# Kernel tuning notes

Hardware: AMD Instinct MI355X
Metric: run time of the kernel (lower is better)

## Reference

```python
import jax, jax.numpy as jnp
import numpy as np
from jax import lax

V, E, H, NL, K = 32000, 1024, 1024, 3, 3
B, T = 16, 1024


def setup_inputs() -> dict:
    key = jax.random.key(0)
    ks = jax.random.split(key, 8)
    return {
        "input_ids": jax.random.randint(ks[0], (B, T), 0, V),
        "attention_mask": jnp.ones((B, T), dtype=jnp.int32),
        "emb": jax.random.normal(ks[1], (V, E), dtype=jnp.float32) * 0.02,
        "convW": jax.random.normal(ks[2], (NL, K, H, 3 * H), dtype=jnp.float32) * 0.02,
        "convb": jnp.zeros((NL, 3 * H), dtype=jnp.float32),
        "gamma": jnp.ones((NL, H), dtype=jnp.float32),
        "beta": jnp.zeros((NL, H), dtype=jnp.float32),
        "W1": jax.random.normal(ks[3], (H, H), dtype=jnp.float32) * 0.02,
        "b1": jnp.zeros((H,), dtype=jnp.float32),
        "W2": jax.random.normal(ks[4], (H, 2), dtype=jnp.float32) * 0.02,
        "b2": jnp.zeros((2,), dtype=jnp.float32),
    }


def _layer_norm(x, g, b, eps=1e-5):
    mu = x.mean(-1, keepdims=True)
    var = ((x - mu) ** 2).mean(-1, keepdims=True)
    return (x - mu) / jnp.sqrt(var + eps) * g + b


def _fo_pool(z, f, o, h0):
    # h_t = o_t * (f_t * h_{t-1} + (1-f_t) * z_t)  ->  h_t = a_t h_{t-1} + b_t
    a = o * f                      # [B,T,H]
    b = o * (1.0 - f) * z          # [B,T,H]
    b = b.at[:, 0].add(a[:, 0] * h0)  # fold initial hidden into first step
    def comb(x, y):
        a1, b1 = x
        a2, b2 = y
        return (a1 * a2, a2 * b1 + b2)
    _, h = lax.associative_scan(comb, (a, b), axis=1)
    return h  # [B,T,H]


def reference(input_ids, attention_mask, emb, convW, convb, gamma, beta, W1, b1, W2, b2):
    x = emb[input_ids]                       # [B,T,E]
    lengths = attention_mask.sum(axis=1)     # [B]
    hidden = jnp.zeros((x.shape[0], H), dtype=x.dtype)
    skips = []
    for i in range(NL):
        # causal conv: left-pad K-1, valid conv == torch pad=K-1 with trailing outputs dropped
        co = lax.conv_general_dilated(
            x, convW[i], window_strides=(1,), padding=[(K - 1, 0)],
            dimension_numbers=("NWC", "WIO", "NWC")) + convb[i]   # [B,T,3H]
        z, f, o = jnp.split(co, 3, axis=-1)
        z = jnp.tanh(z)
        f = jax.nn.sigmoid(f)
        o = jax.nn.sigmoid(o)
        h = _fo_pool(z, f, o, hidden)        # [B,T,H]
        hidden = h[:, -1]                    # pre-layernorm last state feeds next layer
        out = _layer_norm(h, gamma[i], beta[i])
        skips.append(out)
        x = out + skips[-2] if len(skips) > 1 else out
    # dynamic max pool over valid positions
    mask = jnp.arange(T)[None, :] < lengths[:, None]          # [B,T]
    pooled = jnp.where(mask[..., None], x, -jnp.inf).max(axis=1)  # [B,H]
    h1 = jax.nn.relu(pooled @ W1 + b1)
    return h1 @ W2 + b2                       # [B,2]
```

## Files before the change

kernel.cpp:

```cpp
#include <hip/hip_runtime.h>
#include <math.h>


#define B_   16
#define T_   1024
#define TP_  1026
#define H_   1024
#define NL_  3
#define KW   3
#define N3H  3072
#define MTOT (B_ * T_)
#define NSTEP 96


typedef __attribute__((ext_vector_type(8))) __bf16 bfrag;
typedef __attribute__((ext_vector_type(4))) float f32x4;
typedef __attribute__((ext_vector_type(8))) unsigned short us8;
typedef __attribute__((ext_vector_type(4))) unsigned short us4;

typedef unsigned int __attribute__((address_space(1))) gu32;
typedef unsigned int __attribute__((address_space(3))) lu32;

static __device__ __forceinline__ void gl16(const void* g, void* l) {
    __builtin_amdgcn_global_load_lds((const gu32*)g, (lu32*)l, 16, 0, 0);
}
static __device__ __forceinline__ unsigned short f2bf(float x) {
    unsigned int u = __float_as_uint(x);
    u += 0x7fff + ((u >> 16) & 1);
    return (unsigned short)(u >> 16);
}
static __device__ __forceinline__ float bf2f(unsigned short h) {
    return __uint_as_float(((unsigned int)h) << 16);
}

__global__ __launch_bounds__(128) void embed_split_kernel(
    const int* __restrict__ ids, const float* __restrict__ emb,
    char* __restrict__ XHL)
{
    const int tp = blockIdx.x;
    const int b  = blockIdx.y;
    const int tid = threadIdx.x;
    const int c0 = tid * 8;
    char* row = XHL + (size_t)(b * TP_ + tp) * 4096;
    char* hip_ = row + (tid >> 2) * 128 + (tid & 3) * 16;
    if (tp < 2) {
        *(us8*)hip_ = (us8)0;
        *(us8*)(hip_ + 64) = (us8)0;
        return;
    }
    const int id = ids[b * T_ + tp - 2];
    const float* src = emb + (size_t)id * H_ + c0;
    us8 h, l;
#pragma unroll
    for (int j = 0; j < 8; ++j) {
        float x = src[j];
        unsigned short hh = f2bf(x);
        h[j] = hh;
        l[j] = f2bf(x - bf2f(hh));
    }
    *(us8*)hip_ = h;
    *(us8*)(hip_ + 64) = l;
}

__global__ __launch_bounds__(256) void wsplit_kernel(
    const float* __restrict__ W, char* __restrict__ WHL)
{
    __shared__ float t[32][33];
    const int kk = blockIdx.z;
    const int i0 = blockIdx.y * 32;
    const int n0 = blockIdx.x * 32;
    const int r = threadIdx.x >> 3;
    const int c = (threadIdx.x & 7) * 4;
    const float4 v = *(const float4*)(W + ((size_t)kk * H_ + i0 + r) * N3H + n0 + c);
    t[r][c] = v.x; t[r][c + 1] = v.y; t[r][c + 2] = v.z; t[r][c + 3] = v.w;
    __syncthreads();
    char* out = WHL + (size_t)(kk * N3H + n0 + r) * 4096 + (i0 >> 5) * 128 + c * 2;
    us4 h, l;
#pragma unroll
    for (int j = 0; j < 4; ++j) {
        float x = t[c + j][r];
        unsigned short hh = f2bf(x);
        h[j] = hh;
        l[j] = f2bf(x - bf2f(hh));
    }
    *(us4*)out = h;
    *(us4*)(out + 64) = l;
}

__global__ __launch_bounds__(512, 2) void conv_gemm_8ph(
    const char* __restrict__ XHL, const char* __restrict__ WHL,
    const float* __restrict__ bias, float* __restrict__ ZFO)
{
    extern __shared__ char lds[];

    const int tid = threadIdx.x, lane = tid & 63, w = tid >> 6;
    const int wr = w >> 2, wc = w & 3;

    const int id0 = blockIdx.y * gridDim.x + blockIdx.x;
    const int sw  = (id0 & 7) * 96 + (id0 >> 3);
    const int bx = sw % 12, by = sw / 12;
    const int m0 = by * 256, n0 = bx * 256;
    const int batch = m0 >> 10, t0 = m0 & 1023;

    const int rtid = tid >> 3;
    const int swz  = ((lane & 7) ^ (lane >> 3)) << 4;
    const char* Abase = XHL + (size_t)(batch * TP_ + t0) * 4096;

    const int hsw = (((lane >> 4)) ^ (lane & 7)) << 4;
    const int lsw = (((lane >> 4) | 4) ^ (lane & 7)) << 4;
    const int arow = (wr * 128 + (lane & 15)) << 7;
    const int brow = ((wc * 64 + (lane & 15)) << 7) + 32768;

    f32x4 acc[8][4];
#pragma unroll
    for (int m = 0; m < 8; ++m)
#pragma unroll
        for (int n = 0; n < 4; ++n) acc[m][n] = (f32x4)0.f;

#define STAGE_A(bufb, kk, G)                                                  \
    {                                                                         \
        char* ldst = lds + ((bufb) << 16);                                    \
        const char* src = Abase + (size_t)((kk) + rtid) * 4096 + (G) * 128 + swz; \
        _Pragma("unroll")                                                     \
        for (int j = 0; j < 4; ++j)                                           \
            gl16(src + (size_t)j * (64 * 4096), ldst + j * 8192 + tid * 16);  \
    }
#define STAGE_B(bufb, kk, G)                                                  \
    {                                                                         \
        char* ldst = lds + ((bufb) << 16) + 32768;                            \
        const char* src = WHL + (size_t)((kk) * N3H + n0 + rtid) * 4096 + (G) * 128 + swz; \
        _Pragma("unroll")                                                     \
        for (int j = 0; j < 4; ++j)                                           \
            gl16(src + (size_t)j * (64 * 4096), ldst + j * 8192 + tid * 16);  \
    }

    STAGE_A(0, 0, 0);
    STAGE_B(0, 0, 0);
    asm volatile("s_waitcnt vmcnt(0)" ::: "memory");
    __builtin_amdgcn_s_barrier();

    for (int t = 0; t < NSTEP; ++t) {
        const int buf = t & 1;
        const char* L = lds + (buf << 16);
        const int tn = t + 1;
        const int kkn = tn >> 5, Gn = tn & 31;
        const bool more = (t < NSTEP - 1);

#pragma unroll
        for (int p = 0; p < 4; ++p) {
            const int mh = p >> 1, nh = p & 1;
            bfrag ah[4], al[4], bh[2], bl[2];
#pragma unroll
            for (int m = 0; m < 4; ++m) {
                const int ro = arow + ((mh * 4 + m) << 11);
                ah[m] = *(const bfrag*)(L + ro + hsw);
                al[m] = *(const bfrag*)(L + ro + lsw);
            }
#pragma unroll
            for (int n = 0; n < 2; ++n) {
                const int ro = brow + ((nh * 2 + n) << 11);
                bh[n] = *(const bfrag*)(L + ro + hsw);
                bl[n] = *(const bfrag*)(L + ro + lsw);
            }
            if (more && p == 0) STAGE_A(buf ^ 1, kkn, Gn);
            if (more && p == 1) STAGE_B(buf ^ 1, kkn, Gn);

            __builtin_amdgcn_s_barrier();
            asm volatile("s_waitcnt lgkmcnt(0)" ::: "memory");
            __builtin_amdgcn_sched_barrier(0);
            __builtin_amdgcn_s_setprio(1);
#pragma unroll
            for (int m = 0; m < 4; ++m)
#pragma unroll
                for (int n = 0; n < 2; ++n) {
                    f32x4 a0 = acc[mh * 4 + m][nh * 2 + n];
                    a0 = __builtin_amdgcn_mfma_f32_16x16x32_bf16(ah[m], bh[n], a0, 0, 0, 0);
                    a0 = __builtin_amdgcn_mfma_f32_16x16x32_bf16(ah[m], bl[n], a0, 0, 0, 0);
                    a0 = __builtin_amdgcn_mfma_f32_16x16x32_bf16(al[m], bh[n], a0, 0, 0, 0);
                    acc[mh * 4 + m][nh * 2 + n] = a0;
                }
            __builtin_amdgcn_s_setprio(0);
            __builtin_amdgcn_sched_barrier(0);
            if (p == 3) asm volatile("s_waitcnt vmcnt(0)" ::: "memory");
            __builtin_amdgcn_s_barrier();
        }
    }

    const int lcol = lane & 15, lrow = (lane >> 4) * 4;
#pragma unroll
    for (int n4 = 0; n4 < 4; ++n4) {
        const int col = n0 + wc * 64 + n4 * 16 + lcol;
        const float bs = bias[col];
        const int region = col >> 10;
#pragma unroll
        for (int m = 0; m < 8; ++m) {
            const int row = m0 + wr * 128 + m * 16 + lrow;
#pragma unroll
            for (int j = 0; j < 4; ++j) {
                float v = acc[m][n4][j] + bs;
                v = (region == 0) ? tanhf(v) : (1.f / (1.f + expf(-v)));
                ZFO[(size_t)(row + j) * N3H + col] = v;
            }
        }
    }
#undef STAGE_A
#undef STAGE_B
}

__global__ __launch_bounds__(256) void fo_scan_kernel(float* __restrict__ ZFO,
                                                      float* __restrict__ hidden,
                                                      int use_h0)
{
    const int id = blockIdx.x * 256 + threadIdx.x;
    const int b = id >> 10, c = id & 1023;
    float h = use_h0 ? hidden[id] : 0.f;
    float* base = ZFO + (size_t)b * T_ * N3H + c;
    for (int t = 0; t < T_; t += 8) {
        float zv[8], fv[8], ov[8];
#pragma unroll
        for (int u = 0; u < 8; ++u) {
            float* p = base + (size_t)(t + u) * N3H;
            zv[u] = p[0]; fv[u] = p[H_]; ov[u] = p[2 * H_];
        }
#pragma unroll
        for (int u = 0; u < 8; ++u) {
            const float a  = ov[u] * fv[u];
            const float bb = ov[u] * (1.f - fv[u]) * zv[u];
            h = fmaf(a, h, bb);
            base[(size_t)(t + u) * N3H] = h;
        }
    }
    hidden[id] = h;
}

__global__ __launch_bounds__(256) void ln_kernel(
    const float* __restrict__ Hs,
    const float* __restrict__ g, const float* __restrict__ be,
    const float* __restrict__ skip,
    float* __restrict__ OutCur,
    float* __restrict__ Xfin,
    char* __restrict__ XHL,
    int add_skip)
{
    __shared__ float red[8];
    const int row = blockIdx.x;
    const int tid = threadIdx.x;

    const float4 v = *(const float4*)(Hs + (size_t)row * N3H + tid * 4);
    float s  = v.x + v.y + v.z + v.w;
    float s2 = v.x * v.x + v.y * v.y + v.z * v.z + v.w * v.w;
#pragma unroll
    for (int off = 32; off; off >>= 1) {
        s  += __shfl_down(s, off);
        s2 += __shfl_down(s2, off);
    }
    if ((tid & 63) == 0) { red[tid >> 6] = s; red[4 + (tid >> 6)] = s2; }
    __syncthreads();
    s  = red[0] + red[1] + red[2] + red[3];
    s2 = red[4] + red[5] + red[6] + red[7];

    const float mu  = s * (1.f / 1024.f);
    const float var = s2 * (1.f / 1024.f) - mu * mu;
    const float inv = 1.f / sqrtf(var + 1e-5f);

    const float4 gg = *(const float4*)(g  + tid * 4);
    const float4 bb = *(const float4*)(be + tid * 4);
    float4 o;
    o.x = (v.x - mu) * inv * gg.x + bb.x;
    o.y = (v.y - mu) * inv * gg.y + bb.y;
    o.z = (v.z - mu) * inv * gg.z + bb.z;
    o.w = (v.w - mu) * inv * gg.w + bb.w;
    *(float4*)(OutCur + (size_t)row * H_ + tid * 4) = o;

    float4 xn = o;
    if (add_skip) {
        const float4 sk = *(const float4*)(skip + (size_t)row * H_ + tid * 4);
        xn.x += sk.x; xn.y += sk.y; xn.z += sk.z; xn.w += sk.w;
    }
    *(float4*)(Xfin + (size_t)row * N3H + tid * 4) = xn;

    const int b = row >> 10, t = row & 1023;
    char* xrow = XHL + (size_t)(b * TP_ + t + 2) * 4096
               + (tid >> 3) * 128 + (tid & 7) * 8;
    const float xv[4] = {xn.x, xn.y, xn.z, xn.w};
    us4 hh, ll;
#pragma unroll
    for (int j = 0; j < 4; ++j) {
        unsigned short hb = f2bf(xv[j]);
        hh[j] = hb;
        ll[j] = f2bf(xv[j] - bf2f(hb));
    }
    *(us4*)xrow = hh;
    *(us4*)(xrow + 64) = ll;
}

__global__ __launch_bounds__(256) void lengths_kernel(const int* __restrict__ mask,
                                                      int* __restrict__ lengths) {
    __shared__ int red[4];
    const int b = blockIdx.x, tid = threadIdx.x;
    int s = 0;
    for (int k = tid; k < T_; k += 256) s += mask[b * T_ + k];
#pragma unroll
    for (int off = 32; off; off >>= 1) s += __shfl_down(s, off);
    if ((tid & 63) == 0) red[tid >> 6] = s;
    __syncthreads();
    if (tid == 0) lengths[b] = red[0] + red[1] + red[2] + red[3];
}

__global__ __launch_bounds__(256) void maxpool_kernel(const float* __restrict__ Xfin,
                                                      const int* __restrict__ lengths,
                                                      float* __restrict__ pooled) {
    const int id = blockIdx.x * 256 + threadIdx.x;
    const int b = id >> 10, c = id & 1023;
    const int len = lengths[b];
    const float* p = Xfin + (size_t)b * T_ * N3H + c;
    float m = -INFINITY;
    int t = 0;
    for (; t + 8 <= len; t += 8) {
#pragma unroll
        for (int u = 0; u < 8; ++u) m = fmaxf(m, p[(size_t)(t + u) * N3H]);
    }
    for (; t < len; ++t) m = fmaxf(m, p[(size_t)t * N3H]);
    pooled[id] = m;
}

__global__ __launch_bounds__(256) void head1_kernel(const float* __restrict__ pooled,
                                                    const float* __restrict__ W1,
                                                    const float* __restrict__ b1,
                                                    float* __restrict__ h1) {
    const int id = blockIdx.x * 256 + threadIdx.x;
    const int b = id >> 10, j = id & 1023;
    const float* pb = pooled + b * H_;
    float acc = 0.f;
    for (int i = 0; i < H_; i += 8) {
#pragma unroll
        for (int u = 0; u < 8; ++u)
            acc = fmaf(pb[i + u], W1[(size_t)(i + u) * H_ + j], acc);
    }
    h1[id] = fmaxf(acc + b1[j], 0.f);
}

__global__ __launch_bounds__(256) void head2_kernel(const float* __restrict__ h1,
                                                    const float* __restrict__ W2,
                                                    const float* __restrict__ b2,
                                                    float* __restrict__ out) {
    const int tid = threadIdx.x;
    const int oi = tid >> 3;
    const int seg = tid & 7;
    const int b = oi >> 1, jo = oi & 1;
    const float* hb = h1 + b * H_;
    float acc = 0.f;
    const int i0 = seg * 128;
    for (int i = i0; i < i0 + 128; ++i)
        acc = fmaf(hb[i], W2[i * 2 + jo], acc);
    acc += __shfl_down(acc, 4);
    acc += __shfl_down(acc, 2);
    acc += __shfl_down(acc, 1);
    if (seg == 0) out[oi] = acc + b2[jo];
}

extern "C" void kernel_launch(void* const* d_in, const int* in_sizes, int n_in,
                              void* d_out, int out_size, void* d_ws, size_t ws_size,
                              hipStream_t stream) {
    const int*   input_ids = (const int*)d_in[0];
    const int*   attn_mask = (const int*)d_in[1];
    const float* emb   = (const float*)d_in[2];
    const float* convW = (const float*)d_in[3];
    const float* convb = (const float*)d_in[4];
    const float* gamma = (const float*)d_in[5];
    const float* beta  = (const float*)d_in[6];
    const float* W1    = (const float*)d_in[7];
    const float* b1    = (const float*)d_in[8];
    const float* W2    = (const float*)d_in[9];
    const float* b2    = (const float*)d_in[10];

    float* ZFO  = (float*)d_ws;
    float* Out0 = ZFO  + (size_t)MTOT * N3H;
    float* Out1 = Out0 + (size_t)MTOT * H_;
    char*  XHL  = (char*)(Out1 + (size_t)MTOT * H_);
    char*  WHL  = XHL + (size_t)B_ * TP_ * 4096;
    float* hidden  = (float*)(WHL + (size_t)KW * N3H * 4096);
    float* pooled  = hidden + (size_t)B_ * H_;
    float* h1      = pooled + (size_t)B_ * H_;
    int*   lengths = (int*)(h1 + (size_t)B_ * H_);

    hipFuncSetAttribute((const void*)conv_gemm_8ph,
                        hipFuncAttributeMaxDynamicSharedMemorySize, 131072);

    embed_split_kernel<<<dim3(TP_, B_), 128, 0, stream>>>(input_ids, emb, XHL);

    const float* skipPrev = nullptr;
    float* outs[2] = {Out0, Out1};
    for (int l = 0; l < NL_; ++l) {
        wsplit_kernel<<<dim3(N3H / 32, H_ / 32, KW), 256, 0, stream>>>(
            convW + (size_t)l * KW * H_ * N3H, WHL);
        conv_gemm_8ph<<<dim3(12, 64), 512, 131072, stream>>>(
            XHL, WHL, convb + (size_t)l * N3H, ZFO);
        fo_scan_kernel<<<dim3(64), dim3(256), 0, stream>>>(ZFO, hidden, l > 0 ? 1 : 0);
        ln_kernel<<<dim3(MTOT), dim3(256), 0, stream>>>(
            ZFO, gamma + (size_t)l * H_, beta + (size_t)l * H_,
            skipPrev, outs[l & 1], ZFO + H_, XHL, l > 0 ? 1 : 0);
        skipPrev = outs[l & 1];
    }

    lengths_kernel<<<dim3(B_), dim3(256), 0, stream>>>(attn_mask, lengths);
    maxpool_kernel<<<dim3(64), dim3(256), 0, stream>>>(ZFO + H_, lengths, pooled);
    head1_kernel<<<dim3(64), dim3(256), 0, stream>>>(pooled, W1, b1, h1);
    head2_kernel<<<dim3(1), dim3(256), 0, stream>>>(h1, W2, b2, (float*)d_out);
}
```

Measured before the change: 3.120 ms.

## Collapse four-phase GEMM inner loop into a single load-then-compute stage per K-step

```diff
diff --git a/kernel.cpp b/kernel.cpp
--- a/kernel.cpp
+++ b/kernel.cpp
@@ -87,7 +87,7 @@
     *(us4*)(out + 64) = l;
 }
 
-__global__ __launch_bounds__(512, 2) void conv_gemm_8ph(
+__global__ __launch_bounds__(512, 2) void conv_gemm_pipe(
     const char* __restrict__ XHL, const char* __restrict__ WHL,
     const float* __restrict__ bias, float* __restrict__ ZFO)
 {
@@ -136,8 +136,7 @@
 
     STAGE_A(0, 0, 0);
     STAGE_B(0, 0, 0);
-    asm volatile("s_waitcnt vmcnt(0)" ::: "memory");
-    __builtin_amdgcn_s_barrier();
+    __syncthreads();
 
     for (int t = 0; t < NSTEP; ++t) {
         const int buf = t & 1;
@@ -146,44 +145,54 @@
         const int kkn = tn >> 5, Gn = tn & 31;
         const bool more = (t < NSTEP - 1);
 
-#pragma unroll
-        for (int p = 0; p < 4; ++p) {
-            const int mh = p >> 1, nh = p & 1;
-            bfrag ah[4], al[4], bh[2], bl[2];
-#pragma unroll
-            for (int m = 0; m < 4; ++m) {
-                const int ro = arow + ((mh * 4 + m) << 11);
-                ah[m] = *(const bfrag*)(L + ro + hsw);
-                al[m] = *(const bfrag*)(L + ro + lsw);
+        bfrag ah[4], al[4], bh[4], bl[4], a2h[4], a2l[4];
+#pragma unroll
+        for (int m = 0; m < 4; ++m) {
+            const int ro = arow + (m << 11);
+            ah[m] = *(const bfrag*)(L + ro + hsw);
+            al[m] = *(const bfrag*)(L + ro + lsw);
+        }
+#pragma unroll
+        for (int n = 0; n < 4; ++n) {
+            const int ro = brow + (n << 11);
+            bh[n] = *(const bfrag*)(L + ro + hsw);
+            bl[n] = *(const bfrag*)(L + ro + lsw);
+        }
+#pragma unroll
+        for (int m = 0; m < 4; ++m) {
+            const int ro = arow + ((4 + m) << 11);
+            a2h[m] = *(const bfrag*)(L + ro + hsw);
+            a2l[m] = *(const bfrag*)(L + ro + lsw);
+        }
+
+        if (more) { STAGE_A(buf ^ 1, kkn, Gn); STAGE_B(buf ^ 1, kkn, Gn); }
+
+        __builtin_amdgcn_sched_barrier(0);
+
+        __builtin_amdgcn_s_setprio(1);
+#pragma unroll
+        for (int m = 0; m < 4; ++m)
+#pragma unroll
+            for (int n = 0; n < 4; ++n) {
+                f32x4 a0 = acc[m][n];
+                a0 = __builtin_amdgcn_mfma_f32_16x16x32_bf16(ah[m], bh[n], a0, 0, 0, 0);
+                a0 = __builtin_amdgcn_mfma_f32_16x16x32_bf16(ah[m], bl[n], a0, 0, 0, 0);
+                a0 = __builtin_amdgcn_mfma_f32_16x16x32_bf16(al[m], bh[n], a0, 0, 0, 0);
+                acc[m][n] = a0;
             }
 #pragma unroll
-            for (int n = 0; n < 2; ++n) {
-                const int ro = brow + ((nh * 2 + n) << 11);
-                bh[n] = *(const bfrag*)(L + ro + hsw);
-                bl[n] = *(const bfrag*)(L + ro + lsw);
+        for (int m = 0; m < 4; ++m)
+#pragma unroll
+            for (int n = 0; n < 4; ++n) {
+                f32x4 a0 = acc[4 + m][n];
+                a0 = __builtin_amdgcn_mfma_f32_16x16x32_bf16(a2h[m], bh[n], a0, 0, 0, 0);
+                a0 = __builtin_amdgcn_mfma_f32_16x16x32_bf16(a2h[m], bl[n], a0, 0, 0, 0);
+                a0 = __builtin_amdgcn_mfma_f32_16x16x32_bf16(a2l[m], bh[n], a0, 0, 0, 0);
+                acc[4 + m][n] = a0;
             }
-            if (more && p == 0) STAGE_A(buf ^ 1, kkn, Gn);
-            if (more && p == 1) STAGE_B(buf ^ 1, kkn, Gn);
-
-            __builtin_amdgcn_s_barrier();
-            asm volatile("s_waitcnt lgkmcnt(0)" ::: "memory");
-            __builtin_amdgcn_sched_barrier(0);
-            __builtin_amdgcn_s_setprio(1);
-#pragma unroll
-            for (int m = 0; m < 4; ++m)
-#pragma unroll
-                for (int n = 0; n < 2; ++n) {
-                    f32x4 a0 = acc[mh * 4 + m][nh * 2 + n];
-                    a0 = __builtin_amdgcn_mfma_f32_16x16x32_bf16(ah[m], bh[n], a0, 0, 0, 0);
-                    a0 = __builtin_amdgcn_mfma_f32_16x16x32_bf16(ah[m], bl[n], a0, 0, 0, 0);
-                    a0 = __builtin_amdgcn_mfma_f32_16x16x32_bf16(al[m], bh[n], a0, 0, 0, 0);
-                    acc[mh * 4 + m][nh * 2 + n] = a0;
-                }
-            __builtin_amdgcn_s_setprio(0);
-            __builtin_amdgcn_sched_barrier(0);
-            if (p == 3) asm volatile("s_waitcnt vmcnt(0)" ::: "memory");
-            __builtin_amdgcn_s_barrier();
-        }
+        __builtin_amdgcn_s_setprio(0);
+
+        __syncthreads();
     }
 
     const int lcol = lane & 15, lrow = (lane >> 4) * 4;
@@ -384,7 +393,7 @@
     float* h1      = pooled + (size_t)B_ * H_;
     int*   lengths = (int*)(h1 + (size_t)B_ * H_);
 
-    hipFuncSetAttribute((const void*)conv_gemm_8ph,
+    hipFuncSetAttribute((const void*)conv_gemm_pipe,
                         hipFuncAttributeMaxDynamicSharedMemorySize, 131072);
 
     embed_split_kernel<<<dim3(TP_, B_), 128, 0, stream>>>(input_ids, emb, XHL);
@@ -394,7 +403,7 @@
     for (int l = 0; l < NL_; ++l) {
         wsplit_kernel<<<dim3(N3H / 32, H_ / 32, KW), 256, 0, stream>>>(
             convW + (size_t)l * KW * H_ * N3H, WHL);
-        conv_gemm_8ph<<<dim3(12, 64), 512, 131072, stream>>>(
+        conv_gemm_pipe<<<dim3(12, 64), 512, 131072, stream>>>(
             XHL, WHL, convb + (size_t)l * N3H, ZFO);
         fo_scan_kernel<<<dim3(64), dim3(256), 0, stream>>>(ZFO, hidden, l > 0 ? 1 : 0);
         ln_kernel<<<dim3(MTOT), dim3(256), 0, stream>>>(
```

Measured after the change: 2.884 ms. 7.6% less time.
